# Optimization experiments

Measured on AMD Instinct MI355X. Metric: run time of the kernel, lower is better.

## Reference

```python
import jax, jax.numpy as jnp
import numpy as np

B, C, H, W = 256, 3, 224, 224
CROP = 190


def _persp_coeffs(end):
    # torchvision _get_perspective_coeffs: solve for (a..h) with
    # (a*ex+b*ey+c)/(g*ex+h*ey+1)=sx, (d*ex+e*ey+f)/(g*ex+h*ey+1)=sy
    start = jnp.array([[0., 0.], [223., 0.], [223., 223.], [0., 223.]], jnp.float32)
    ex, ey = end[:, 0], end[:, 1]
    sx, sy = start[:, 0], start[:, 1]
    o = jnp.ones(4, jnp.float32); z = jnp.zeros(4, jnp.float32)
    r1 = jnp.stack([ex, ey, o, z, z, z, -sx * ex, -sx * ey], axis=-1)
    r2 = jnp.stack([z, z, z, ex, ey, o, -sy * ex, -sy * ey], axis=-1)
    A = jnp.concatenate([r1, r2], axis=0)  # [8,8]
    b = jnp.concatenate([sx, sy], axis=0)
    return jnp.linalg.solve(A, b)


def _bilinear(img, sx, sy):
    # img [C,H,W]; sx,sy [H,W] source index coords; zero padding outside.
    Hh, Ww = img.shape[-2], img.shape[-1]
    x0 = jnp.floor(sx); y0 = jnp.floor(sy)
    wx = sx - x0; wy = sy - y0
    x0i = x0.astype(jnp.int32); y0i = y0.astype(jnp.int32)

    def tap(yi, xi, w):
        valid = ((xi >= 0) & (xi < Ww) & (yi >= 0) & (yi < Hh)).astype(img.dtype)
        v = img[:, jnp.clip(yi, 0, Hh - 1), jnp.clip(xi, 0, Ww - 1)]
        return v * (w * valid)[None]

    return (tap(y0i, x0i, (1 - wx) * (1 - wy)) + tap(y0i, x0i + 1, wx * (1 - wy))
            + tap(y0i + 1, x0i, (1 - wx) * wy) + tap(y0i + 1, x0i + 1, wx * wy))


def _augment(x, noise, brightness, flip_mask, ep_raw, angles, crop_ij):
    Bb, Cc, Hh, Ww = x.shape
    # random hflip
    x = jnp.where(flip_mask[:, None, None, None] > 0, x[..., ::-1], x)
    # gaussian noise (std 0.625) and brightness in [0.85, 1.15]
    x = x + 0.625 * noise
    x = x * (0.85 + 0.30 * brightness)[:, None, None, None]
    # batched perspective warp (bilinear, zero fill)
    offs = jnp.array([[0., 0.], [195., 0.], [195., 195.], [0., 195.]], jnp.float32)
    end = ep_raw.astype(jnp.float32) + offs  # [B,4,2] endpoints
    coeffs = jax.vmap(_persp_coeffs)(end)    # [B,8]
    Xg, Yg = jnp.meshgrid(jnp.arange(Ww, dtype=jnp.float32) + 0.5,
                          jnp.arange(Hh, dtype=jnp.float32) + 0.5, indexing='xy')
    a, b, c, d, e, f, g, h = [coeffs[:, i][:, None, None] for i in range(8)]
    den = g * Xg + h * Yg + 1.0
    sx = (a * Xg + b * Yg + c) / den - 0.5  # half-pixel centers, align_corners=False
    sy = (d * Xg + e * Yg + f) / den - 0.5
    x = jax.vmap(_bilinear)(x, sx, sy)
    # batched rotation about image center (bilinear, zero fill)
    th = (angles.astype(jnp.float32) - 16.0) * (jnp.pi / 180.0)
    cos = jnp.cos(th)[:, None, None]; sin = jnp.sin(th)[:, None, None]
    cx = (Ww - 1) / 2.0; cy = (Hh - 1) / 2.0
    dx = (Xg - 0.5) - cx; dy = (Yg - 0.5) - cy
    rx = cos * dx + sin * dy + cx
    ry = -sin * dx + cos * dy + cy
    x = jax.vmap(_bilinear)(x, rx, ry)
    # per-sample 190x190 crop
    x = jax.vmap(lambda img, ij: jax.lax.dynamic_slice(
        img, (0, ij[0], ij[1]), (Cc, CROP, CROP)))(x, crop_ij)
    # bicubic resize back to 224x224
    x = jax.image.resize(x, (Bb, Cc, Hh, Ww), method='bicubic')
    return x


def setup_inputs() -> dict:
    key = jax.random.key(0)
    ks = jax.random.split(key, 7)
    return {
        'x': jax.random.uniform(ks[0], (B, C, H, W), dtype=jnp.float32),
        'noise': jax.random.normal(ks[1], (B, C, H, W), dtype=jnp.float32),
        'brightness': jax.random.uniform(ks[2], (B,), dtype=jnp.float32),
        'flip_mask': jax.random.randint(ks[3], (B,), 0, 2, dtype=jnp.int32),
        'ep_raw': jax.random.randint(ks[4], (B, 4, 2), 0, 29, dtype=jnp.int32),
        'angles': jax.random.randint(ks[5], (B,), 0, 33, dtype=jnp.int32),
        'crop_ij': jax.random.randint(ks[6], (B, 2), 0, 35, dtype=jnp.int32),
    }


def reference(x, noise, brightness, flip_mask, ep_raw, angles, crop_ij):
    return _augment(x, noise, brightness, flip_mask, ep_raw, angles, crop_ij)
```

## Files before the change

### kernel.cpp

```cpp
#include <hip/hip_runtime.h>
#include <math.h>

#define Bn 256
#define Cn 3
#define Hn 224
#define Wn 224
#define CROPD 190

static constexpr int PLANE = Hn * Wn;

#define TILE 32
#define FH 72
#define FSTR 76
#define PHR 48
#define PSTR 52
#define RSTR 40

#define NWG (768 * 49)
#define CHUNK (NWG / 8)

__device__ int    g_i0[Wn];
__device__ float4 g_wt[Wn];

__device__ __forceinline__ float keys_cubic(float x) {
    if (x < 1.f) return ((1.5f * x - 2.5f) * x) * x + 1.f;
    if (x < 2.f) return ((-0.5f * x + 2.5f) * x - 4.f) * x + 2.f;
    return 0.f;
}
__device__ __forceinline__ float rflf(float v) {
    return __int_as_float(__builtin_amdgcn_readfirstlane(__float_as_int(v)));
}
__device__ __forceinline__ int rfli(int v) { return __builtin_amdgcn_readfirstlane(v); }
__device__ __forceinline__ int swz_block(int bid) {
    return (bid & 7) * CHUNK + (bid >> 3);
}

__global__ void params_kernel(const int* __restrict__ ep_raw,
                              const int* __restrict__ angles,
                              const float* __restrict__ brightness,
                              const int* __restrict__ flip_mask,
                              float* __restrict__ params) {
    int b = threadIdx.x;

    if (b < Wn) {
        float sf = ((float)b + 0.5f) * ((float)CROPD / (float)Wn) - 0.5f;
        int i0 = (int)floorf(sf);
        float w[4]; float s = 0.f;
#pragma unroll
        for (int k = 0; k < 4; k++) {
            int idx = i0 - 1 + k;
            float wk = (idx >= 0 && idx < CROPD) ? keys_cubic(fabsf(sf - (float)idx)) : 0.f;
            w[k] = wk; s += wk;
        }
        float inv = 1.f / s;
        g_i0[b] = i0;
        g_wt[b] = make_float4(w[0] * inv, w[1] * inv, w[2] * inv, w[3] * inv);
    }

    if (b >= Bn) return;

    const double offx[4] = {0.0, 195.0, 195.0, 0.0};
    const double offy[4] = {0.0, 0.0, 195.0, 195.0};
    const double sxc[4]  = {0.0, 223.0, 223.0, 0.0};
    const double syc[4]  = {0.0, 0.0, 223.0, 223.0};
    double M[8][9];
    for (int i = 0; i < 4; i++) {
        double ex = (double)ep_raw[b * 8 + i * 2 + 0] + offx[i];
        double ey = (double)ep_raw[b * 8 + i * 2 + 1] + offy[i];
        double sx = sxc[i], sy = syc[i];
        M[i][0] = ex; M[i][1] = ey; M[i][2] = 1.0;
        M[i][3] = 0.0; M[i][4] = 0.0; M[i][5] = 0.0;
        M[i][6] = -sx * ex; M[i][7] = -sx * ey; M[i][8] = sx;
        M[i + 4][0] = 0.0; M[i + 4][1] = 0.0; M[i + 4][2] = 0.0;
        M[i + 4][3] = ex; M[i + 4][4] = ey; M[i + 4][5] = 1.0;
        M[i + 4][6] = -sy * ex; M[i + 4][7] = -sy * ey; M[i + 4][8] = sy;
    }
    for (int k = 0; k < 8; k++) {
        int piv = k; double best = fabs(M[k][k]);
        for (int r = k + 1; r < 8; r++) {
            double v = fabs(M[r][k]);
            if (v > best) { best = v; piv = r; }
        }
        if (piv != k)
            for (int j = 0; j < 9; j++) { double tt = M[k][j]; M[k][j] = M[piv][j]; M[piv][j] = tt; }
        double inv = 1.0 / M[k][k];
        for (int r = k + 1; r < 8; r++) {
            double f = M[r][k] * inv;
            M[r][k] = 0.0;
            for (int j = k + 1; j < 9; j++) M[r][j] -= f * M[k][j];
        }
    }
    double sol[8];
    for (int k = 7; k >= 0; k--) {
        double s = M[k][8];
        for (int j = k + 1; j < 8; j++) s -= M[k][j] * sol[j];
        sol[k] = s / M[k][k];
    }
    float* p = params + b * 12;
    for (int j = 0; j < 8; j++) p[j] = (float)sol[j];
    double th = ((double)angles[b] - 16.0) * (M_PI / 180.0);
    p[8]  = (float)cos(th);
    p[9]  = (float)sin(th);
    p[10] = 0.85f + 0.3f * brightness[b];
    p[11] = (flip_mask[b] > 0) ? 1.0f : 0.0f;
}

__global__ void meta_kernel(const float* __restrict__ params,
                            const int* __restrict__ crop_ij,
                            int4* __restrict__ rmeta,
                            int4* __restrict__ smeta) {
    int bt = blockIdx.x * 256 + threadIdx.x;
    int b = bt / 49, t = bt % 49;
    int ty = (t / 7) * TILE, tx = (t % 7) * TILE;
    const float* prm = params + b * 12;

    int x0p, y0p, bwp, bhp;
    {
        float cs = prm[8], sn = prm[9];
        int ci = crop_ij[b * 2 + 0], cj = crop_ij[b * 2 + 1];
        int iymin = max(g_i0[ty] - 1, 0);
        int iymax = min(g_i0[ty + 31] + 2, CROPD - 1);
        int jmin = max(g_i0[tx] - 1, 0);
        int jmax = min(g_i0[tx + 31] + 2, CROPD - 1);
        int ry0 = iymin + ci, ry1 = iymax + ci;
        int rx0 = jmin + cj, rx1 = jmax + cj;
        const float cxc = (Wn - 1) * 0.5f;
        float minrx = 1e30f, maxrx = -1e30f, minry = 1e30f, maxry = -1e30f;
#pragma unroll
        for (int cy = 0; cy < 2; cy++) {
#pragma unroll
            for (int cxr = 0; cxr < 2; cxr++) {
                float dx = (float)(cxr ? rx1 : rx0) - cxc;
                float dy = (float)(cy ? ry1 : ry0) - cxc;
                float rx = cs * dx + sn * dy + cxc;
                float ry = -sn * dx + cs * dy + cxc;
                minrx = fminf(minrx, rx); maxrx = fmaxf(maxrx, rx);
                minry = fminf(minry, ry); maxry = fmaxf(maxry, ry);
            }
        }
        int x0b = min(max((int)floorf(minrx) - 1, 0), Wn - 1);
        int x1b = min(max((int)floorf(maxrx) + 2, 0), Wn - 1);
        int y0b = min(max((int)floorf(minry) - 1, 0), Hn - 1);
        int y1b = min(max((int)floorf(maxry) + 2, 0), Hn - 1);
        x0p = x0b; y0p = y0b;
        bwp = x1b - x0b + 1; bhp = y1b - y0b + 1;
        int inter = (minrx >= 0.5f && maxrx <= 222.0f &&
                     minry >= 0.5f && maxry <= 222.0f) ? 1 : 0;
        rmeta[bt] = make_int4(x0b, y0b, bwp | (inter << 16), bhp);
    }

    {
        float a0 = prm[0], a1 = prm[1], a2 = prm[2];
        float a3 = prm[3], a4 = prm[4], a5 = prm[5];
        float g = prm[6], h = prm[7];
        int x1p = x0p + bwp - 1, y1p = y0p + bhp - 1;
        float minsx = 1e30f, maxsx = -1e30f, minsy = 1e30f, maxsy = -1e30f;
#pragma unroll
        for (int cy = 0; cy < 2; cy++) {
#pragma unroll
            for (int cxr = 0; cxr < 2; cxr++) {
                float Xg = (float)(cxr ? x1p : x0p) + 0.5f;
                float Yg = (float)(cy ? y1p : y0p) + 0.5f;
                float rden = 1.0f / (g * Xg + h * Yg + 1.0f);
                float sx = (a0 * Xg + a1 * Yg + a2) * rden - 0.5f;
                float sy = (a3 * Xg + a4 * Yg + a5) * rden - 0.5f;
                minsx = fminf(minsx, sx); maxsx = fmaxf(maxsx, sx);
                minsy = fminf(minsy, sy); maxsy = fmaxf(maxsy, sy);
            }
        }
        int x0s = min(max((int)floorf(minsx) - 1, 0), Wn - 1);
        int x1s = min(max((int)floorf(maxsx) + 2, 0), Wn - 1);
        int y0s = min(max((int)floorf(minsy) - 1, 0), Hn - 1);
        int y1s = min(max((int)floorf(maxsy) + 2, 0), Hn - 1);
        x0s &= ~3;
        int bws = x1s - x0s + 1, bhs = y1s - y0s + 1;
        int inter = (minsx >= 0.5f && maxsx <= 222.0f &&
                     minsy >= 0.5f && maxsy <= 222.0f) ? 1 : 0;
        smeta[bt] = make_int4(x0s, y0s, bws | (inter << 16), bhs);
    }
}

__device__ __forceinline__ float persp_at(const float* __restrict__ xb,
                                          const float* __restrict__ nb,
                                          bool flip, float bf,
                                          float a0, float a1, float a2,
                                          float a3, float a4, float a5,
                                          float g, float h, int ixp, int iyp) {
    float Xg = (float)ixp + 0.5f, Yg = (float)iyp + 0.5f;
    float rden = __builtin_amdgcn_rcpf(g * Xg + h * Yg + 1.0f);
    float sx = (a0 * Xg + a1 * Yg + a2) * rden - 0.5f;
    float sy = (a3 * Xg + a4 * Yg + a5) * rden - 0.5f;
    float fx0 = floorf(sx), fy0 = floorf(sy);
    float wx = sx - fx0, wy = sy - fy0;
    int x0 = (int)fx0, y0 = (int)fy0;
    float acc = 0.f;
#pragma unroll
    for (int dy = 0; dy < 2; dy++) {
        int yy = y0 + dy;
        float wyv = dy ? wy : 1.f - wy;
        bool yv = (unsigned)yy < (unsigned)Hn;
        int yc = min(max(yy, 0), Hn - 1);
#pragma unroll
        for (int dx = 0; dx < 2; dx++) {
            int xx = x0 + dx;
            float wxv = dx ? wx : 1.f - wx;
            bool v = yv && ((unsigned)xx < (unsigned)Wn);
            int xc = min(max(xx, 0), Wn - 1);
            float wgt = v ? wxv * wyv : 0.f;
            int xs = flip ? (Wn - 1 - xc) : xc;
            acc += (xb[yc * Wn + xs] + 0.625f * nb[yc * Wn + xc]) * bf * wgt;
        }
    }
    return acc;
}

__global__ __launch_bounds__(256) void mega_kernel(const float* __restrict__ xin,
                                                   const float* __restrict__ noise,
                                                   const float* __restrict__ params,
                                                   const int* __restrict__ crop_ij,
                                                   const int4* __restrict__ rmeta,
                                                   const int4* __restrict__ smeta,
                                                   float* __restrict__ out) {
    __shared__ __align__(16) float smem[FH * FSTR + PHR * PSTR];
    float* Flds = smem;
    float* Plds = smem + FH * FSTR;
    float* Rlds = smem;
    float* Tlds = smem + 32 * RSTR;

    int bi = swz_block(blockIdx.x);
    int p = bi / 49;
    int t = bi % 49;
    int ty = (t / 7) * TILE;
    int tx = (t % 7) * TILE;
    int b = p / Cn;
    int tid = threadIdx.x;

    int4 rm = rmeta[b * 49 + t];
    int x0p = rm.x, y0p = rm.y;
    int bwp = rm.z & 0xffff;
    bool interior_r = (rm.z >> 16) != 0;
    int bhp = rm.w;
    int4 sm = smeta[b * 49 + t];
    int x0s = sm.x, y0s = sm.y;
    int bws = sm.z & 0xffff;
    bool interior_s = (sm.z >> 16) != 0;
    int bhs = sm.w;
    int y1s = y0s + bhs - 1;
    bool fitF = (bws <= FH) && (bhs <= FH);
    bool fitP = (bwp <= PHR) && (bhp <= PHR);
    bool fast = fitF && fitP;

    const float* prm = params + b * 12;
    float a0 = rflf(prm[0]), a1 = rflf(prm[1]), a2 = rflf(prm[2]);
    float a3 = rflf(prm[3]), a4 = rflf(prm[4]), a5 = rflf(prm[5]);
    float g = rflf(prm[6]), h = rflf(prm[7]), bf = rflf(prm[10]);
    float cs = rflf(prm[8]), sn = rflf(prm[9]);
    bool flip = rflf(prm[11]) > 0.5f;
    int ci = rfli(crop_ij[b * 2 + 0]);
    int cj = rfli(crop_ij[b * 2 + 1]);

    int iymin = max(g_i0[ty] - 1, 0);
    int nTy = min(g_i0[ty + 31] + 2, CROPD - 1) - iymin + 1;
    int jmin = max(g_i0[tx] - 1, 0);
    int nRx = min(g_i0[tx + 31] + 2, CROPD - 1) - jmin + 1;
    int rx0 = jmin + cj, ry0 = iymin + ci;
    const float cxc = (Wn - 1) * 0.5f;

    const size_t base = (size_t)p * PLANE;
    const float* xb = xin + base;
    const float* nb = noise + base;

    if (fast) {
        int bwq = (bws + 3) >> 2;
        int sh = (bwq <= 8) ? 3 : ((bwq <= 16) ? 4 : 5);
        int c4 = tid & ((1 << sh) - 1);
        int r0 = tid >> sh;
        int rstep = 256 >> sh;
        bool cok = c4 < bwq;
        for (int yy = y0s + r0; yy <= y1s; yy += rstep) {
            if (cok) {
                int xl = min(x0s + c4 * 4, Wn - 4);
                float4 nv = *reinterpret_cast<const float4*>(&nb[yy * Wn + xl]);
                float4 xv;
                if (flip) {
                    float4 xr = *reinterpret_cast<const float4*>(&xb[yy * Wn + (Wn - 4 - xl)]);
                    xv = make_float4(xr.w, xr.z, xr.y, xr.x);
                } else {
                    xv = *reinterpret_cast<const float4*>(&xb[yy * Wn + xl]);
                }
                float4 f = make_float4((xv.x + 0.625f * nv.x) * bf,
                                       (xv.y + 0.625f * nv.y) * bf,
                                       (xv.z + 0.625f * nv.z) * bf,
                                       (xv.w + 0.625f * nv.w) * bf);
                *reinterpret_cast<float4*>(&Flds[(yy - y0s) * FSTR + (xl - x0s)]) = f;
            }
        }
    }
    __syncthreads();

    if (fast) {
        int bwpq = (bwp + 3) >> 2;
        int c4 = tid & 15;
        int r0 = tid >> 4;
        bool cok = c4 < bwpq;
        int x1p = x0p + bwp - 1;
        if (interior_s) {
            for (int pr = r0; pr < bhp; pr += 16) {
                if (!cok) continue;
                float Yg = (float)(y0p + pr) + 0.5f;
                float pv[4];
#pragma unroll
                for (int j = 0; j < 4; j++) {
                    int px = min(x0p + c4 * 4 + j, x1p);
                    float Xg = (float)px + 0.5f;
                    float rden = __builtin_amdgcn_rcpf(g * Xg + h * Yg + 1.0f);
                    float sx = (a0 * Xg + a1 * Yg + a2) * rden - 0.5f;
                    float sy = (a3 * Xg + a4 * Yg + a5) * rden - 0.5f;
                    float fx0 = floorf(sx), fy0 = floorf(sy);
                    float wx = sx - fx0, wy = sy - fy0;
                    const float* q = &Flds[((int)fy0 - y0s) * FSTR + ((int)fx0 - x0s)];
                    float top = q[0] + wx * (q[1] - q[0]);
                    float bot = q[FSTR] + wx * (q[FSTR + 1] - q[FSTR]);
                    pv[j] = top + wy * (bot - top);
                }
                *reinterpret_cast<float4*>(&Plds[pr * PSTR + c4 * 4]) =
                    make_float4(pv[0], pv[1], pv[2], pv[3]);
            }
        } else {
            for (int pr = r0; pr < bhp; pr += 16) {
                if (!cok) continue;
                float Yg = (float)(y0p + pr) + 0.5f;
                float pv[4];
#pragma unroll
                for (int j = 0; j < 4; j++) {
                    int px = min(x0p + c4 * 4 + j, x1p);
                    float Xg = (float)px + 0.5f;
                    float rden = __builtin_amdgcn_rcpf(g * Xg + h * Yg + 1.0f);
                    float sx = (a0 * Xg + a1 * Yg + a2) * rden - 0.5f;
                    float sy = (a3 * Xg + a4 * Yg + a5) * rden - 0.5f;
                    float fx0 = floorf(sx), fy0 = floorf(sy);
                    float wx = sx - fx0, wy = sy - fy0;
                    int x0 = (int)fx0, y0 = (int)fy0;
                    float acc = 0.f;
#pragma unroll
                    for (int dy = 0; dy < 2; dy++) {
                        int yy = y0 + dy;
                        float wyv = dy ? wy : 1.f - wy;
                        bool yv = (unsigned)yy < (unsigned)Hn;
                        int yc = min(max(yy, 0), Hn - 1);
#pragma unroll
                        for (int dx = 0; dx < 2; dx++) {
                            int xx = x0 + dx;
                            float wxv = dx ? wx : 1.f - wx;
                            bool v = yv && ((unsigned)xx < (unsigned)Wn);
                            int xc = min(max(xx, 0), Wn - 1);
                            float wgt = v ? wxv * wyv : 0.f;
                            acc += Flds[(yc - y0s) * FSTR + (xc - x0s)] * wgt;
                        }
                    }
                    pv[j] = acc;
                }
                *reinterpret_cast<float4*>(&Plds[pr * PSTR + c4 * 4]) =
                    make_float4(pv[0], pv[1], pv[2], pv[3]);
            }
        }
    }
    __syncthreads();

    {
        int rc = tid & 31;
        int rbase = tid >> 5;
        bool cok = rc < nRx;
        float dxc = (float)(rx0 + rc) - cxc;
        float bx = cs * dxc + cxc;
        float by = -sn * dxc + cxc;
        if (fast && interior_r) {
#pragma unroll
            for (int it = 0; it < 4; it++) {
                int rr = it * 8 + rbase;
                if (rr < nTy && cok) {
                    float dyr = (float)(ry0 + rr) - cxc;
                    float srx = bx + sn * dyr;
                    float sry = by + cs * dyr;
                    float fx0 = floorf(srx), fy0 = floorf(sry);
                    float wx = srx - fx0, wy = sry - fy0;
                    const float* q = &Plds[((int)fy0 - y0p) * PSTR + ((int)fx0 - x0p)];
                    float top = q[0] + wx * (q[1] - q[0]);
                    float bot = q[PSTR] + wx * (q[PSTR + 1] - q[PSTR]);
                    Rlds[rr * RSTR + rc] = top + wy * (bot - top);
                }
            }
        } else if (fast) {
#pragma unroll
            for (int it = 0; it < 4; it++) {
                int rr = it * 8 + rbase;
                if (rr < nTy && cok) {
                    float dyr = (float)(ry0 + rr) - cxc;
                    float srx = bx + sn * dyr;
                    float sry = by + cs * dyr;
                    float fx0 = floorf(srx), fy0 = floorf(sry);
                    float wx = srx - fx0, wy = sry - fy0;
                    int x0 = (int)fx0, y0 = (int)fy0;
                    float acc = 0.f;
#pragma unroll
                    for (int ddy = 0; ddy < 2; ddy++) {
                        int yy = y0 + ddy;
                        float wyv = ddy ? wy : 1.f - wy;
                        bool yv = (unsigned)yy < (unsigned)Hn;
                        int yc = min(max(yy, 0), Hn - 1);
#pragma unroll
                        for (int ddx = 0; ddx < 2; ddx++) {
                            int xx = x0 + ddx;
                            float wxv = ddx ? wx : 1.f - wx;
                            bool v = yv && ((unsigned)xx < (unsigned)Wn);
                            int xc = min(max(xx, 0), Wn - 1);
                            float wgt = v ? wxv * wyv : 0.f;
                            acc += Plds[(yc - y0p) * PSTR + (xc - x0p)] * wgt;
                        }
                    }
                    Rlds[rr * RSTR + rc] = acc;
                }
            }
        } else {
#pragma unroll
            for (int it = 0; it < 4; it++) {
                int rr = it * 8 + rbase;
                if (rr < nTy && cok) {
                    float dyr = (float)(ry0 + rr) - cxc;
                    float srx = bx + sn * dyr;
                    float sry = by + cs * dyr;
                    float fx0 = floorf(srx), fy0 = floorf(sry);
                    float wx = srx - fx0, wy = sry - fy0;
                    int x0 = (int)fx0, y0 = (int)fy0;
                    float acc = 0.f;
#pragma unroll
                    for (int ddy = 0; ddy < 2; ddy++) {
                        int yy = y0 + ddy;
                        float wyv = ddy ? wy : 1.f - wy;
                        bool yv = (unsigned)yy < (unsigned)Hn;
                        int yc = min(max(yy, 0), Hn - 1);
#pragma unroll
                        for (int ddx = 0; ddx < 2; ddx++) {
                            int xx = x0 + ddx;
                            float wxv = ddx ? wx : 1.f - wx;
                            bool v = yv && ((unsigned)xx < (unsigned)Wn);
                            int xc = min(max(xx, 0), Wn - 1);
                            float wgt = v ? wxv * wyv : 0.f;
                            if (wgt != 0.f)
                                acc += persp_at(xb, nb, flip, bf, a0, a1, a2,
                                                a3, a4, a5, g, h, xc, yc) * wgt;
                        }
                    }
                    Rlds[rr * RSTR + rc] = acc;
                }
            }
        }
    }
    __syncthreads();

    {
        int oc = tid & 31;
        int rbase = tid >> 5;
        int ox = tx + oc;
        float4 w = g_wt[ox];
        int j0 = g_i0[ox];
        int jc0 = min(max(j0 - 1, 0), CROPD - 1) - jmin;
        int jc1 = min(max(j0 + 0, 0), CROPD - 1) - jmin;
        int jc2 = min(max(j0 + 1, 0), CROPD - 1) - jmin;
        int jc3 = min(max(j0 + 2, 0), CROPD - 1) - jmin;
#pragma unroll
        for (int it = 0; it < 4; it++) {
            int rr = it * 8 + rbase;
            if (rr < nTy) {
                const float* row = &Rlds[rr * RSTR];
                Tlds[rr * RSTR + oc] = w.x * row[jc0] + w.y * row[jc1] +
                                       w.z * row[jc2] + w.w * row[jc3];
            }
        }
    }
    __syncthreads();

    {
        int r = tid >> 3, cg = tid & 7;
        int oy = ty + r, ox0 = tx + cg * 4;
        float4 w = g_wt[oy];
        int i0y = g_i0[oy];
        float wk[4] = {w.x, w.y, w.z, w.w};
        float4 acc = make_float4(0.f, 0.f, 0.f, 0.f);
#pragma unroll
        for (int k = 0; k < 4; k++) {
            int iyc = min(max(i0y - 1 + k, 0), CROPD - 1) - iymin;
            float4 v = *reinterpret_cast<const float4*>(&Tlds[iyc * RSTR + cg * 4]);
            acc.x += wk[k] * v.x;
            acc.y += wk[k] * v.y;
            acc.z += wk[k] * v.z;
            acc.w += wk[k] * v.w;
        }
        *reinterpret_cast<float4*>(out + base + (size_t)oy * Wn + ox0) = acc;
    }
}

extern "C" void kernel_launch(void* const* d_in, const int* in_sizes, int n_in,
                              void* d_out, int out_size, void* d_ws, size_t ws_size,
                              hipStream_t stream) {
    const float* x          = (const float*)d_in[0];
    const float* noise      = (const float*)d_in[1];
    const float* brightness = (const float*)d_in[2];
    const int*   flip_mask  = (const int*)d_in[3];
    const int*   ep_raw     = (const int*)d_in[4];
    const int*   angles     = (const int*)d_in[5];
    const int*   crop_ij    = (const int*)d_in[6];
    float* out = (float*)d_out;

    float* params = (float*)d_ws;
    int4*  rmeta  = (int4*)((char*)d_ws + 16384);
    int4*  smeta  = (int4*)((char*)d_ws + 16384 + 200704);

    params_kernel<<<1, 256, 0, stream>>>(ep_raw, angles, brightness, flip_mask, params);
    meta_kernel<<<49, 256, 0, stream>>>(params, crop_ij, rmeta, smeta);
    mega_kernel<<<NWG, 256, 0, stream>>>(x, noise, params, crop_ij, rmeta, smeta, out);
}
```

Measured before the change: 270.9 us.

## Flatten LDS staging loops, incrementalize projective math, shrink P tile for occupancy

The global-to-LDS staging and perspective-stage loops now map a flat element index to (row, col) with a magic-multiply division, instead of fixed power-of-two column groups that left threads idle. The projective numerator and denominator are stepped incrementally across the four pixels rather than recomputed. floorf is replaced by int truncation in the interior paths, which assumes non-negative coordinates. The P tile is shrunk and launch bounds request five blocks per CU to raise occupancy, at the cost of more tiles falling back to the slow path when they exceed the smaller P buffer.

```diff
diff --git a/kernel.cpp b/kernel.cpp
--- a/kernel.cpp
+++ b/kernel.cpp
@@ -12,8 +12,8 @@
 #define TILE 32
 #define FH 72
 #define FSTR 76
-#define PHR 48
-#define PSTR 52
+#define PHR 44
+#define PSTR 48
 #define RSTR 40
 
 #define NWG (768 * 49)
@@ -214,13 +214,13 @@
     return acc;
 }
 
-__global__ __launch_bounds__(256) void mega_kernel(const float* __restrict__ xin,
-                                                   const float* __restrict__ noise,
-                                                   const float* __restrict__ params,
-                                                   const int* __restrict__ crop_ij,
-                                                   const int4* __restrict__ rmeta,
-                                                   const int4* __restrict__ smeta,
-                                                   float* __restrict__ out) {
+__global__ __launch_bounds__(256, 5) void mega_kernel(const float* __restrict__ xin,
+                                                      const float* __restrict__ noise,
+                                                      const float* __restrict__ params,
+                                                      const int* __restrict__ crop_ij,
+                                                      const int4* __restrict__ rmeta,
+                                                      const int4* __restrict__ smeta,
+                                                      float* __restrict__ out) {
     __shared__ __align__(16) float smem[FH * FSTR + PHR * PSTR];
     float* Flds = smem;
     float* Plds = smem + FH * FSTR;
@@ -245,7 +245,6 @@
     int bws = sm.z & 0xffff;
     bool interior_s = (sm.z >> 16) != 0;
     int bhs = sm.w;
-    int y1s = y0s + bhs - 1;
     bool fitF = (bws <= FH) && (bhs <= FH);
     bool fitP = (bwp <= PHR) && (bhp <= PHR);
     bool fast = fitF && fitP;
@@ -272,72 +271,75 @@
 
     if (fast) {
         int bwq = (bws + 3) >> 2;
-        int sh = (bwq <= 8) ? 3 : ((bwq <= 16) ? 4 : 5);
-        int c4 = tid & ((1 << sh) - 1);
-        int r0 = tid >> sh;
-        int rstep = 256 >> sh;
-        bool cok = c4 < bwq;
-        for (int yy = y0s + r0; yy <= y1s; yy += rstep) {
-            if (cok) {
-                int xl = min(x0s + c4 * 4, Wn - 4);
-                float4 nv = *reinterpret_cast<const float4*>(&nb[yy * Wn + xl]);
-                float4 xv;
-                if (flip) {
-                    float4 xr = *reinterpret_cast<const float4*>(&xb[yy * Wn + (Wn - 4 - xl)]);
-                    xv = make_float4(xr.w, xr.z, xr.y, xr.x);
-                } else {
-                    xv = *reinterpret_cast<const float4*>(&xb[yy * Wn + xl]);
-                }
-                float4 f = make_float4((xv.x + 0.625f * nv.x) * bf,
-                                       (xv.y + 0.625f * nv.y) * bf,
-                                       (xv.z + 0.625f * nv.z) * bf,
-                                       (xv.w + 0.625f * nv.w) * bf);
-                *reinterpret_cast<float4*>(&Flds[(yy - y0s) * FSTR + (xl - x0s)]) = f;
-            }
+        unsigned Mf = (1u << 20) / (unsigned)bwq + 1;
+        int tot = bhs * bwq;
+        for (int e = tid; e < tot; e += 256) {
+            int fr = (int)(((unsigned)e * Mf) >> 20);
+            int fc = e - fr * bwq;
+            int yy = y0s + fr;
+            int xl = min(x0s + fc * 4, Wn - 4);
+            float4 nv = *reinterpret_cast<const float4*>(&nb[yy * Wn + xl]);
+            float4 xv;
+            if (flip) {
+                float4 xr = *reinterpret_cast<const float4*>(&xb[yy * Wn + (Wn - 4 - xl)]);
+                xv = make_float4(xr.w, xr.z, xr.y, xr.x);
+            } else {
+                xv = *reinterpret_cast<const float4*>(&xb[yy * Wn + xl]);
+            }
+            float4 f = make_float4((xv.x + 0.625f * nv.x) * bf,
+                                   (xv.y + 0.625f * nv.y) * bf,
+                                   (xv.z + 0.625f * nv.z) * bf,
+                                   (xv.w + 0.625f * nv.w) * bf);
+            *reinterpret_cast<float4*>(&Flds[fr * FSTR + (xl - x0s)]) = f;
         }
     }
     __syncthreads();
 
     if (fast) {
         int bwpq = (bwp + 3) >> 2;
-        int c4 = tid & 15;
-        int r0 = tid >> 4;
-        bool cok = c4 < bwpq;
-        int x1p = x0p + bwp - 1;
+        unsigned Mp = (1u << 20) / (unsigned)bwpq + 1;
+        int tot = bhp * bwpq;
         if (interior_s) {
-            for (int pr = r0; pr < bhp; pr += 16) {
-                if (!cok) continue;
+            for (int e = tid; e < tot; e += 256) {
+                int pr = (int)(((unsigned)e * Mp) >> 20);
+                int pc = e - pr * bwpq;
                 float Yg = (float)(y0p + pr) + 0.5f;
+                float Xg0 = (float)(x0p + pc * 4) + 0.5f;
+                float nx = a0 * Xg0 + (a1 * Yg + a2);
+                float ny = a3 * Xg0 + (a4 * Yg + a5);
+                float dn = g * Xg0 + (h * Yg + 1.0f);
                 float pv[4];
 #pragma unroll
                 for (int j = 0; j < 4; j++) {
-                    int px = min(x0p + c4 * 4 + j, x1p);
-                    float Xg = (float)px + 0.5f;
-                    float rden = __builtin_amdgcn_rcpf(g * Xg + h * Yg + 1.0f);
-                    float sx = (a0 * Xg + a1 * Yg + a2) * rden - 0.5f;
-                    float sy = (a3 * Xg + a4 * Yg + a5) * rden - 0.5f;
-                    float fx0 = floorf(sx), fy0 = floorf(sy);
-                    float wx = sx - fx0, wy = sy - fy0;
-                    const float* q = &Flds[((int)fy0 - y0s) * FSTR + ((int)fx0 - x0s)];
+                    float r = __builtin_amdgcn_rcpf(dn);
+                    float sx = nx * r - 0.5f;
+                    float sy = ny * r - 0.5f;
+                    int ix = (int)sx; float wx = sx - (float)ix;
+                    int iy = (int)sy; float wy = sy - (float)iy;
+                    const float* q = &Flds[(iy - y0s) * FSTR + (ix - x0s)];
                     float top = q[0] + wx * (q[1] - q[0]);
                     float bot = q[FSTR] + wx * (q[FSTR + 1] - q[FSTR]);
                     pv[j] = top + wy * (bot - top);
+                    nx += a0; ny += a3; dn += g;
                 }
-                *reinterpret_cast<float4*>(&Plds[pr * PSTR + c4 * 4]) =
+                *reinterpret_cast<float4*>(&Plds[pr * PSTR + pc * 4]) =
                     make_float4(pv[0], pv[1], pv[2], pv[3]);
             }
         } else {
-            for (int pr = r0; pr < bhp; pr += 16) {
-                if (!cok) continue;
+            for (int e = tid; e < tot; e += 256) {
+                int pr = (int)(((unsigned)e * Mp) >> 20);
+                int pc = e - pr * bwpq;
                 float Yg = (float)(y0p + pr) + 0.5f;
+                float Xg0 = (float)(x0p + pc * 4) + 0.5f;
+                float nx = a0 * Xg0 + (a1 * Yg + a2);
+                float ny = a3 * Xg0 + (a4 * Yg + a5);
+                float dn = g * Xg0 + (h * Yg + 1.0f);
                 float pv[4];
 #pragma unroll
                 for (int j = 0; j < 4; j++) {
-                    int px = min(x0p + c4 * 4 + j, x1p);
-                    float Xg = (float)px + 0.5f;
-                    float rden = __builtin_amdgcn_rcpf(g * Xg + h * Yg + 1.0f);
-                    float sx = (a0 * Xg + a1 * Yg + a2) * rden - 0.5f;
-                    float sy = (a3 * Xg + a4 * Yg + a5) * rden - 0.5f;
+                    float r = __builtin_amdgcn_rcpf(dn);
+                    float sx = nx * r - 0.5f;
+                    float sy = ny * r - 0.5f;
                     float fx0 = floorf(sx), fy0 = floorf(sy);
                     float wx = sx - fx0, wy = sy - fy0;
                     int x0 = (int)fx0, y0 = (int)fy0;
@@ -359,8 +361,9 @@
                         }
                     }
                     pv[j] = acc;
+                    nx += a0; ny += a3; dn += g;
                 }
-                *reinterpret_cast<float4*>(&Plds[pr * PSTR + c4 * 4]) =
+                *reinterpret_cast<float4*>(&Plds[pr * PSTR + pc * 4]) =
                     make_float4(pv[0], pv[1], pv[2], pv[3]);
             }
         }
@@ -382,9 +385,9 @@
                     float dyr = (float)(ry0 + rr) - cxc;
                     float srx = bx + sn * dyr;
                     float sry = by + cs * dyr;
-                    float fx0 = floorf(srx), fy0 = floorf(sry);
-                    float wx = srx - fx0, wy = sry - fy0;
-                    const float* q = &Plds[((int)fy0 - y0p) * PSTR + ((int)fx0 - x0p)];
+                    int ix = (int)srx; float wx = srx - (float)ix;
+                    int iy = (int)sry; float wy = sry - (float)iy;
+                    const float* q = &Plds[(iy - y0p) * PSTR + (ix - x0p)];
                     float top = q[0] + wx * (q[1] - q[0]);
                     float bot = q[PSTR] + wx * (q[PSTR + 1] - q[PSTR]);
                     Rlds[rr * RSTR + rc] = top + wy * (bot - top);
```

Result: faster. 249.5 us (-7.9%).
